# Kernel optimization log

Measured on AMD Instinct MI355X. Metric: run time of the kernel, lower is better.

## Reference

```python
import jax, jax.numpy as jnp
import numpy as np

H, C = 4, 32  # heads, per-head channels
EPS = 1e-5


def setup_inputs() -> dict:
    key = jax.random.key(0)
    ks = jax.random.split(key, 12)
    N, E, IN = 100000, 1600000, 16
    lut_idx = jnp.arange(1024, dtype=jnp.int32)
    x = jax.random.normal(ks[0], (N, IN), dtype=jnp.float32)
    # LUT flag column: exactly the lut_idx nodes have value 1.0 (matches x[:,15]==1.0 mask)
    x = x.at[:, 15].set(0.0).at[lut_idx, 15].set(1.0)
    edge_index = jax.random.randint(ks[1], (2, E), 0, N, dtype=jnp.int64)
    s = 0.1
    return {
        "x": x,
        "edge_index": edge_index,
        "lut_idx": lut_idx,
        "W_lin": jax.random.normal(ks[2], (IN, H * C), dtype=jnp.float32) * s,
        "att_src": jax.random.normal(ks[3], (H, C), dtype=jnp.float32) * s,
        "att_dst": jax.random.normal(ks[4], (H, C), dtype=jnp.float32) * s,
        "bias_gat": jnp.zeros((H * C,), dtype=jnp.float32),
        "gamma": jnp.ones((H * C,), dtype=jnp.float32),
        "beta": jnp.zeros((H * C,), dtype=jnp.float32),
        "W1": jax.random.normal(ks[5], (H * C, 32), dtype=jnp.float32) * s,
        "b1": jnp.zeros((32,), dtype=jnp.float32),
        "W2": jax.random.normal(ks[6], (32, 1), dtype=jnp.float32) * s,
        "b2": jnp.zeros((1,), dtype=jnp.float32),
    }


def gat_conv(x, edge_index, W_lin, att_src, att_dst, bias_gat):
    N = x.shape[0]
    # add self-loops (PyG GATConv default)
    loops = jnp.arange(N, dtype=edge_index.dtype)
    src = jnp.concatenate([edge_index[0], loops])
    dst = jnp.concatenate([edge_index[1], loops])
    h = (x @ W_lin).reshape(N, H, C)                      # [N,H,C]
    a_src = (h * att_src[None]).sum(-1)                   # [N,H]
    a_dst = (h * att_dst[None]).sum(-1)                   # [N,H]
    e = jax.nn.leaky_relu(a_src[src] + a_dst[dst], 0.2)   # [Etot,H]
    m = jax.ops.segment_max(e, dst, num_segments=N)       # stable softmax per dst
    e = jnp.exp(e - m[dst])
    denom = jax.ops.segment_sum(e, dst, num_segments=N)
    alpha = e / denom[dst]                                # [Etot,H]
    msg = h[src] * alpha[:, :, None]                      # [Etot,H,C]
    out = jax.ops.segment_sum(msg, dst, num_segments=N)   # [N,H,C]
    return out.reshape(N, H * C) + bias_gat


def reference(x, edge_index, lut_idx, W_lin, att_src, att_dst, bias_gat,
              gamma, beta, W1, b1, W2, b2):
    h = gat_conv(x, edge_index, W_lin, att_src, att_dst, bias_gat)
    # BatchNorm over nodes (training-mode batch stats, biased var, eps=1e-5)
    mean = h.mean(axis=0)
    var = h.var(axis=0)
    h = (h - mean) / jnp.sqrt(var + EPS) * gamma + beta
    h = jax.nn.relu(h)
    emb = h[lut_idx]                                      # masked LUT nodes
    z = jax.nn.leaky_relu(emb @ W1 + b1, 0.01)            # Dropout is identity in eval
    out = z @ W2 + b2                                     # [n_lut, 1]
    return jnp.squeeze(out, axis=0) if out.shape[0] == 1 else out
```

## Files before the change

kernel.cpp:

```cpp
#include <hip/hip_runtime.h>
#include <hip/hip_fp16.h>
#include <cstdint>
#include <cstring>

typedef unsigned int uint;

#define BSHIFT 8
#define NBUCK 512
#define TILE 4096
#define SCAT_T 512
#define SORT_T 512
#define SORT_CAP 5120

__device__ __forceinline__ float leaky02(float x) { return x > 0.f ? x : 0.2f * x; }
__device__ __forceinline__ float bflo(uint u) { return __uint_as_float(u << 16); }
__device__ __forceinline__ float bfhi(uint u) { return __uint_as_float(u & 0xffff0000u); }

__device__ __forceinline__ uint pack_bf16x2(float a, float b) {
    uint ua = __float_as_uint(a), ub = __float_as_uint(b);
    ua += 0x7fffu + ((ua >> 16) & 1u);
    ub += 0x7fffu + ((ub >> 16) & 1u);
    return (ua >> 16) | (ub & 0xffff0000u);
}

__device__ __forceinline__ uint packh2(float a, float b) {
    __half ha = __float2half_rn(a), hb = __float2half_rn(b);
    unsigned short ua, ub;
    memcpy(&ua, &ha, 2);
    memcpy(&ub, &hb, 2);
    return (uint)ua | ((uint)ub << 16);
}

__global__ void k_prep(const float* __restrict__ W, const float* __restrict__ att_s,
                       const float* __restrict__ att_d, float* __restrict__ WsWd,
                       int* __restrict__ cursor, float* __restrict__ sums,
                       float* __restrict__ sumsq) {
    int t = threadIdx.x;
    cursor[t] = 0; cursor[t + 128] = 0; cursor[t + 256] = 0; cursor[t + 384] = 0;
    sums[t] = 0.f; sumsq[t] = 0.f;
    if (t < 64) {
        int k = t >> 2, hh = t & 3;
        float s1 = 0.f, s2 = 0.f;
        for (int c = 0; c < 32; c++) {
            float wv = W[k * 128 + hh * 32 + c];
            s1 += wv * att_s[hh * 32 + c];
            s2 += wv * att_d[hh * 32 + c];
        }
        WsWd[t] = s1;
        WsWd[64 + t] = s2;
    }
}

__global__ void k_linear(const float* __restrict__ x, const float* __restrict__ W,
                         const float* __restrict__ WsWd,
                         uint* __restrict__ h, float* __restrict__ a_src,
                         float* __restrict__ a_dst, int N) {
    int tid = threadIdx.x;
    __shared__ float sx[32][16];
    __shared__ float sWs[64], sWd[64];
    int j = tid & 63;
    int sub = tid >> 6;
    int n0 = blockIdx.x * 32;

    float2 wreg[16];
#pragma unroll
    for (int k = 0; k < 16; k++) wreg[k] = ((const float2*)(W + k * 128))[j];

    if (tid < 128) {
        int row = tid >> 2;
        if (n0 + row < N)
            ((float4*)sx)[tid] = ((const float4*)(x + (size_t)n0 * 16))[tid];
    } else if (tid < 192) {
        sWs[tid - 128] = WsWd[tid - 128];
    } else {
        sWd[tid - 192] = WsWd[64 + (tid - 192)];
    }
    __syncthreads();

#pragma unroll
    for (int i = 0; i < 8; i++) {
        int loc = sub + i * 4;
        int n = n0 + loc;
        if (n >= N) break;
        float acc0 = 0.f, acc1 = 0.f;
#pragma unroll
        for (int k = 0; k < 16; k++) {
            float xk = sx[loc][k];
            acc0 += xk * wreg[k].x;
            acc1 += xk * wreg[k].y;
        }
        h[(size_t)n * 64 + j] = pack_bf16x2(acc0, acc1);
    }

    int loc2 = tid >> 3, hh = (tid >> 1) & 3, sd = tid & 1;
    int n2 = n0 + loc2;
    if (n2 < N) {
        const float* Wm = sd ? sWd : sWs;
        float acc = 0.f;
#pragma unroll
        for (int k = 0; k < 16; k++) acc += sx[loc2][k] * Wm[k * 4 + hh];
        if (sd) a_dst[n2 * 4 + hh] = acc;
        else    a_src[n2 * 4 + hh] = acc;
    }
}

__global__ void kb_scatter(const int* __restrict__ src, const int* __restrict__ dst, int E,
                           int* __restrict__ cursor, uint* __restrict__ pairs) {
    __shared__ int tileCnt[NBUCK], tileCnt2[NBUCK], tileOff[NBUCK], gbase[NBUCK];
    __shared__ int wsum[8], wbase[8];
    __shared__ uint lp[TILE];
    __shared__ unsigned short lb[TILE];
    int tid = threadIdx.x;
    int l = tid & 63, w = tid >> 6;
    int t0 = blockIdx.x * TILE;
    tileCnt[tid] = 0;
    tileCnt2[tid] = 0;
    __syncthreads();
    int dreg[8], sreg[8];
#pragma unroll
    for (int j = 0; j < 8; j++) {
        int idx = t0 + j * SCAT_T + tid;
        if (idx < E) {
            dreg[j] = dst[idx];
            sreg[j] = src[idx];
            atomicAdd(&tileCnt[dreg[j] >> BSHIFT], 1);
        } else dreg[j] = -1;
    }
    __syncthreads();
    int v = tileCnt[tid];
    int s = v;
#pragma unroll
    for (int off = 1; off < 64; off <<= 1) {
        int t = __shfl_up(s, off);
        if (l >= off) s += t;
    }
    if (l == 63) wsum[w] = s;
    __syncthreads();
    if (tid < 8) {
        int b = 0;
        for (int i = 0; i < tid; i++) b += wsum[i];
        wbase[tid] = b;
    }
    __syncthreads();
    int ex = s - v + wbase[w];
    tileOff[tid] = ex;
    if (v > 0) gbase[tid] = atomicAdd(&cursor[tid], v);
    __syncthreads();
#pragma unroll
    for (int j = 0; j < 8; j++) {
        if (dreg[j] >= 0) {
            int bk = dreg[j] >> BSHIFT;
            int r = atomicAdd(&tileCnt2[bk], 1);
            int pos = tileOff[bk] + r;
            lp[pos] = ((uint)sreg[j] << BSHIFT) | (uint)(dreg[j] & 255);
            lb[pos] = (unsigned short)bk;
        }
    }
    __syncthreads();
    int tot = min(TILE, E - t0);
    for (int k = tid; k < tot; k += SCAT_T) {
        int bk = lb[k];
        int lpos = gbase[bk] + (k - tileOff[bk]);
        if (lpos < SORT_CAP)
            pairs[(size_t)bk * SORT_CAP + lpos] = lp[k];
    }
}

__global__ void kb_sort(const uint* __restrict__ pairs, const int* __restrict__ cursor,
                        const float* __restrict__ a_src, const float* __restrict__ a_dst,
                        int N,
                        int* __restrict__ sorted, uint2* __restrict__ wsorted,
                        int* __restrict__ offsets, int* __restrict__ degs) {
    __shared__ int cnt[256], off0[256];
    __shared__ int wsum[4], wbase[4];
    __shared__ uint lcode[SORT_CAP];
    __shared__ float4 sad[256];
    int tid = threadIdx.x;
    int l = tid & 63, w = tid >> 6;
    int b = blockIdx.x;
    int n0 = b << BSHIFT;
    int nn = min(256, N - n0);
    int ebase = b * SORT_CAP;
    int ecnt = cursor[b];
    if (ecnt > SORT_CAP) ecnt = SORT_CAP;
    if (tid < 256) cnt[tid] = 0;
    if (tid < nn) sad[tid] = ((const float4*)a_dst)[n0 + tid];
    __syncthreads();
    for (int k = tid; k < ecnt; k += SORT_T)
        atomicAdd(&cnt[pairs[ebase + k] & 255], 1);
    __syncthreads();
    int v = (tid < 256) ? cnt[tid] : 0;
    int s = v;
#pragma unroll
    for (int off = 1; off < 64; off <<= 1) {
        int t = __shfl_up(s, off);
        if (l >= off) s += t;
    }
    if (tid < 256 && l == 63) wsum[w] = s;
    __syncthreads();
    if (tid < 4) {
        int base = 0;
        for (int i = 0; i < tid; i++) base += wsum[i];
        wbase[tid] = base;
    }
    __syncthreads();
    if (tid < 256) off0[tid] = s - v + wbase[w];
    __syncthreads();
    if (tid < 256) cnt[tid] = 0;
    __syncthreads();
    for (int k = tid; k < ecnt; k += SORT_T) {
        uint p = pairs[ebase + k];
        int ln = p & 255;
        int r = atomicAdd(&cnt[ln], 1);
        lcode[off0[ln] + r] = p;
    }
    __syncthreads();
    for (int k = tid; k < ecnt; k += SORT_T) {
        uint p = lcode[k];
        int src = (int)(p >> BSHIFT);
        int ln = p & 255;
        sorted[ebase + k] = src;
        float4 as = ((const float4*)a_src)[src];
        float4 ad = sad[ln];
        float w0 = __expf(leaky02(as.x + ad.x));
        float w1 = __expf(leaky02(as.y + ad.y));
        float w2 = __expf(leaky02(as.z + ad.z));
        float w3 = __expf(leaky02(as.w + ad.w));
        wsorted[ebase + k] = make_uint2(packh2(w0, w1), packh2(w2, w3));
    }
    if (tid < nn) {
        offsets[n0 + tid] = ebase + off0[tid];
        degs[n0 + tid] = v;
    }
}

__global__ void k_gat(const int* __restrict__ offsets, const int* __restrict__ degs,
                      const int* __restrict__ sorted, const uint2* __restrict__ wsorted,
                      const uint* __restrict__ h, const float* __restrict__ a_src,
                      const float* __restrict__ a_dst, const float* __restrict__ bias,
                      uint* __restrict__ hagg, int N) {
    int nb = gridDim.x;
    int g = nb >> 3;
    int bi = blockIdx.x;
    int blk = (bi < (g << 3)) ? ((bi & 7) * g + (bi >> 3)) : bi;
    int lane = threadIdx.x & 63;
    int wid = threadIdx.x >> 6;
    int q = lane >> 4;
    int l16 = lane & 15;
    int head = l16 >> 2;
    int d = blk * 16 + wid * 4 + q;
    if (d >= N) return;
    int base = offsets[d];
    int deg = degs[d];

    const int* sp = sorted + base;
    const __half* wp = (const __half*)(wsorted + base) + head;

    float w = __expf(leaky02(a_src[d * 4 + head] + a_dst[d * 4 + head]));
    uint4 u = ((const uint4*)(h + (size_t)d * 64))[l16];
    float sum = w;
    float2 a01 = make_float2(w * bflo(u.x), w * bfhi(u.x));
    float2 a23 = make_float2(w * bflo(u.y), w * bfhi(u.y));
    float2 a45 = make_float2(w * bflo(u.z), w * bfhi(u.z));
    float2 a67 = make_float2(w * bflo(u.w), w * bfhi(u.w));

    int i = 0;
    for (; i + 3 < deg; i += 4) {
        int s0 = sp[i];
        int s1 = sp[i + 1];
        int s2 = sp[i + 2];
        int s3 = sp[i + 3];
        float w0 = __half2float(wp[i * 4]);
        float w1 = __half2float(wp[(i + 1) * 4]);
        float w2 = __half2float(wp[(i + 2) * 4]);
        float w3 = __half2float(wp[(i + 3) * 4]);
        uint4 u0 = ((const uint4*)(h + (size_t)s0 * 64))[l16];
        uint4 u1 = ((const uint4*)(h + (size_t)s1 * 64))[l16];
        uint4 u2 = ((const uint4*)(h + (size_t)s2 * 64))[l16];
        uint4 u3 = ((const uint4*)(h + (size_t)s3 * 64))[l16];
        sum += (w0 + w1) + (w2 + w3);
        float2 w02 = {w0, w0}, w12 = {w1, w1}, w22 = {w2, w2}, w32 = {w3, w3};
        a01 += make_float2(bflo(u0.x), bfhi(u0.x)) * w02
             + make_float2(bflo(u1.x), bfhi(u1.x)) * w12
             + make_float2(bflo(u2.x), bfhi(u2.x)) * w22
             + make_float2(bflo(u3.x), bfhi(u3.x)) * w32;
        a23 += make_float2(bflo(u0.y), bfhi(u0.y)) * w02
             + make_float2(bflo(u1.y), bfhi(u1.y)) * w12
             + make_float2(bflo(u2.y), bfhi(u2.y)) * w22
             + make_float2(bflo(u3.y), bfhi(u3.y)) * w32;
        a45 += make_float2(bflo(u0.z), bfhi(u0.z)) * w02
             + make_float2(bflo(u1.z), bfhi(u1.z)) * w12
             + make_float2(bflo(u2.z), bfhi(u2.z)) * w22
             + make_float2(bflo(u3.z), bfhi(u3.z)) * w32;
        a67 += make_float2(bflo(u0.w), bfhi(u0.w)) * w02
             + make_float2(bflo(u1.w), bfhi(u1.w)) * w12
             + make_float2(bflo(u2.w), bfhi(u2.w)) * w22
             + make_float2(bflo(u3.w), bfhi(u3.w)) * w32;
    }
    for (; i < deg; i++) {
        int s0 = sp[i];
        float w0 = __half2float(wp[i * 4]);
        uint4 u0 = ((const uint4*)(h + (size_t)s0 * 64))[l16];
        sum += w0;
        float2 w02 = {w0, w0};
        a01 += make_float2(bflo(u0.x), bfhi(u0.x)) * w02;
        a23 += make_float2(bflo(u0.y), bfhi(u0.y)) * w02;
        a45 += make_float2(bflo(u0.z), bfhi(u0.z)) * w02;
        a67 += make_float2(bflo(u0.w), bfhi(u0.w)) * w02;
    }
    float inv = 1.f / sum;
    float4 b0 = ((const float4*)bias)[2 * l16];
    float4 b1 = ((const float4*)bias)[2 * l16 + 1];
    uint4 o;
    o.x = pack_bf16x2(a01.x * inv + b0.x, a01.y * inv + b0.y);
    o.y = pack_bf16x2(a23.x * inv + b0.z, a23.y * inv + b0.w);
    o.z = pack_bf16x2(a45.x * inv + b1.x, a45.y * inv + b1.y);
    o.w = pack_bf16x2(a67.x * inv + b1.z, a67.y * inv + b1.w);
    ((uint4*)(hagg + (size_t)d * 64))[l16] = o;
}

__global__ void k_bnstats(const uint* __restrict__ hagg, int N,
                          float* __restrict__ sums, float* __restrict__ sumsq) {
    int t = threadIdx.x;
    int cg = t & 31, rs = t >> 5;
    float4 s = make_float4(0.f, 0.f, 0.f, 0.f), q = make_float4(0.f, 0.f, 0.f, 0.f);
    for (int n = blockIdx.x * 8 + rs; n < N; n += gridDim.x * 8) {
        uint2 u = ((const uint2*)(hagg + (size_t)n * 64))[cg];
        float v0 = bflo(u.x), v1 = bfhi(u.x), v2 = bflo(u.y), v3 = bfhi(u.y);
        s.x += v0; s.y += v1; s.z += v2; s.w += v3;
        q.x += v0 * v0; q.y += v1 * v1; q.z += v2 * v2; q.w += v3 * v3;
    }
    __shared__ float4 ls[256], lq[256];
    ls[t] = s; lq[t] = q;
    __syncthreads();
    if (t < 32) {
        float4 S = ls[t], Q = lq[t];
        for (int r = 1; r < 8; r++) {
            float4 a = ls[t + r * 32], b = lq[t + r * 32];
            S.x += a.x; S.y += a.y; S.z += a.z; S.w += a.w;
            Q.x += b.x; Q.y += b.y; Q.z += b.z; Q.w += b.w;
        }
        atomicAdd(&sums[t * 4 + 0], S.x);
        atomicAdd(&sums[t * 4 + 1], S.y);
        atomicAdd(&sums[t * 4 + 2], S.z);
        atomicAdd(&sums[t * 4 + 3], S.w);
        atomicAdd(&sumsq[t * 4 + 0], Q.x);
        atomicAdd(&sumsq[t * 4 + 1], Q.y);
        atomicAdd(&sumsq[t * 4 + 2], Q.z);
        atomicAdd(&sumsq[t * 4 + 3], Q.w);
    }
}

__global__ void k_mlp(const uint* __restrict__ hagg, const int* __restrict__ lut,
                      const float* __restrict__ sums, const float* __restrict__ sumsq,
                      const float* __restrict__ gamma, const float* __restrict__ beta,
                      const float* __restrict__ W1, const float* __restrict__ b1,
                      const float* __restrict__ W2, const float* __restrict__ b2,
                      float* __restrict__ out, int N, int nlut) {
    int blk = blockIdx.x;
    if (blk >= nlut) return;
    int node = lut[blk];
    int lane = threadIdx.x;
    __shared__ float v[128];
    float invN = 1.f / (float)N;
    uint u = hagg[(size_t)node * 64 + lane];
    int c0 = 2 * lane, c1 = 2 * lane + 1;
    {
        float mean = sums[c0] * invN;
        float var = sumsq[c0] * invN - mean * mean;
        float val = (bflo(u) - mean) / sqrtf(var + 1e-5f) * gamma[c0] + beta[c0];
        v[c0] = fmaxf(val, 0.f);
        mean = sums[c1] * invN;
        var = sumsq[c1] * invN - mean * mean;
        val = (bfhi(u) - mean) / sqrtf(var + 1e-5f) * gamma[c1] + beta[c1];
        v[c1] = fmaxf(val, 0.f);
    }
    __syncthreads();
    float r = 0.f;
    if (lane < 32) {
        float z = b1[lane];
        for (int c = 0; c < 128; c++) z += v[c] * W1[c * 32 + lane];
        z = z > 0.f ? z : 0.01f * z;
        r = z * W2[lane];
    }
#pragma unroll
    for (int off = 16; off >= 1; off >>= 1) r += __shfl_xor(r, off);
    if (lane == 0) out[blk] = r + b2[0];
}

extern "C" void kernel_launch(void* const* d_in, const int* in_sizes, int n_in,
                              void* d_out, int out_size, void* d_ws, size_t ws_size,
                              hipStream_t stream) {
    const float* x     = (const float*)d_in[0];
    const int*   edges = (const int*)d_in[1];
    const int*   lut   = (const int*)d_in[2];
    const float* W_lin = (const float*)d_in[3];
    const float* att_s = (const float*)d_in[4];
    const float* att_d = (const float*)d_in[5];
    const float* bias  = (const float*)d_in[6];
    const float* gamma = (const float*)d_in[7];
    const float* beta  = (const float*)d_in[8];
    const float* W1    = (const float*)d_in[9];
    const float* b1    = (const float*)d_in[10];
    const float* W2    = (const float*)d_in[11];
    const float* b2    = (const float*)d_in[12];

    int N = in_sizes[0] / 16;
    int E = in_sizes[1] / 2;
    int nlut = in_sizes[2];
    int B = (N + 255) >> BSHIFT;

    const int* esrc = edges;
    const int* edst = edges + E;

    char* ws = (char*)d_ws;
    size_t off = 0;
    auto alloc = [&](size_t bytes) -> void* {
        void* p = ws + off;
        off += (bytes + 255) & ~(size_t)255;
        return p;
    };
    uint*  h       = (uint*)alloc((size_t)N * 64 * 4);
    uint*  hagg    = (uint*)alloc((size_t)N * 64 * 4);
    float* a_src   = (float*)alloc((size_t)N * 4 * 4);
    float* a_dst   = (float*)alloc((size_t)N * 4 * 4);
    int*   offsets = (int*)alloc((size_t)N * 4);
    int*   degs    = (int*)alloc((size_t)N * 4);
    int*   sorted  = (int*)alloc((size_t)B * SORT_CAP * 4);
    uint2* wsorted = (uint2*)alloc((size_t)B * SORT_CAP * 8);
    uint*  pairs   = (uint*)alloc((size_t)B * SORT_CAP * 4);
    int*   cursor  = (int*)alloc((size_t)NBUCK * 4);
    float* sums    = (float*)alloc(128 * 4);
    float* sumsq   = (float*)alloc(128 * 4);
    float* WsWd    = (float*)alloc(128 * 4);

    k_prep<<<1, 128, 0, stream>>>(W_lin, att_s, att_d, WsWd, cursor, sums, sumsq);
    k_linear<<<(N + 31) / 32, 256, 0, stream>>>(x, W_lin, WsWd, h, a_src, a_dst, N);
    kb_scatter<<<(E + TILE - 1) / TILE, SCAT_T, 0, stream>>>(esrc, edst, E, cursor, pairs);
    kb_sort<<<B, SORT_T, 0, stream>>>(pairs, cursor, a_src, a_dst, N,
                                      sorted, wsorted, offsets, degs);
    k_gat<<<(N + 15) / 16, 256, 0, stream>>>(offsets, degs, sorted, wsorted, h,
                                             a_src, a_dst, bias, hagg, N);
    k_bnstats<<<256, 256, 0, stream>>>(hagg, N, sums, sumsq);
    k_mlp<<<nlut, 64, 0, stream>>>(hagg, lut, sums, sumsq, gamma, beta, W1, b1, W2, b2,
                                   (float*)d_out, N, nlut);
}
```

Baseline: 237.8 us.

## Recompute attention weights in GAT gather instead of precomputing them in sort

```diff
diff --git a/kernel.cpp b/kernel.cpp
--- a/kernel.cpp
+++ b/kernel.cpp
@@ -1,5 +1,4 @@
 #include <hip/hip_runtime.h>
-#include <hip/hip_fp16.h>
 #include <cstdint>
 #include <cstring>
 
@@ -21,14 +20,6 @@
     ua += 0x7fffu + ((ua >> 16) & 1u);
     ub += 0x7fffu + ((ub >> 16) & 1u);
     return (ua >> 16) | (ub & 0xffff0000u);
-}
-
-__device__ __forceinline__ uint packh2(float a, float b) {
-    __half ha = __float2half_rn(a), hb = __float2half_rn(b);
-    unsigned short ua, ub;
-    memcpy(&ua, &ha, 2);
-    memcpy(&ub, &hb, 2);
-    return (uint)ua | ((uint)ub << 16);
 }
 
 __global__ void k_prep(const float* __restrict__ W, const float* __restrict__ att_s,
@@ -167,14 +158,10 @@
 }
 
 __global__ void kb_sort(const uint* __restrict__ pairs, const int* __restrict__ cursor,
-                        const float* __restrict__ a_src, const float* __restrict__ a_dst,
-                        int N,
-                        int* __restrict__ sorted, uint2* __restrict__ wsorted,
+                        int N, int* __restrict__ sorted,
                         int* __restrict__ offsets, int* __restrict__ degs) {
     __shared__ int cnt[256], off0[256];
     __shared__ int wsum[4], wbase[4];
-    __shared__ uint lcode[SORT_CAP];
-    __shared__ float4 sad[256];
     int tid = threadIdx.x;
     int l = tid & 63, w = tid >> 6;
     int b = blockIdx.x;
@@ -184,7 +171,6 @@
     int ecnt = cursor[b];
     if (ecnt > SORT_CAP) ecnt = SORT_CAP;
     if (tid < 256) cnt[tid] = 0;
-    if (tid < nn) sad[tid] = ((const float4*)a_dst)[n0 + tid];
     __syncthreads();
     for (int k = tid; k < ecnt; k += SORT_T)
         atomicAdd(&cnt[pairs[ebase + k] & 255], 1);
@@ -212,21 +198,7 @@
         uint p = pairs[ebase + k];
         int ln = p & 255;
         int r = atomicAdd(&cnt[ln], 1);
-        lcode[off0[ln] + r] = p;
-    }
-    __syncthreads();
-    for (int k = tid; k < ecnt; k += SORT_T) {
-        uint p = lcode[k];
-        int src = (int)(p >> BSHIFT);
-        int ln = p & 255;
-        sorted[ebase + k] = src;
-        float4 as = ((const float4*)a_src)[src];
-        float4 ad = sad[ln];
-        float w0 = __expf(leaky02(as.x + ad.x));
-        float w1 = __expf(leaky02(as.y + ad.y));
-        float w2 = __expf(leaky02(as.z + ad.z));
-        float w3 = __expf(leaky02(as.w + ad.w));
-        wsorted[ebase + k] = make_uint2(packh2(w0, w1), packh2(w2, w3));
+        sorted[ebase + off0[ln] + r] = (int)(p >> BSHIFT);
     }
     if (tid < nn) {
         offsets[n0 + tid] = ebase + off0[tid];
@@ -234,8 +206,9 @@
     }
 }
 
-__global__ void k_gat(const int* __restrict__ offsets, const int* __restrict__ degs,
-                      const int* __restrict__ sorted, const uint2* __restrict__ wsorted,
+__global__ void __launch_bounds__(256) k_gat(
+                      const int* __restrict__ offsets, const int* __restrict__ degs,
+                      const int* __restrict__ sorted,
                       const uint* __restrict__ h, const float* __restrict__ a_src,
                       const float* __restrict__ a_dst, const float* __restrict__ bias,
                       uint* __restrict__ hagg, int N) {
@@ -254,9 +227,9 @@
     int deg = degs[d];
 
     const int* sp = sorted + base;
-    const __half* wp = (const __half*)(wsorted + base) + head;
-
-    float w = __expf(leaky02(a_src[d * 4 + head] + a_dst[d * 4 + head]));
+
+    float ad = a_dst[d * 4 + head];
+    float w = __expf(leaky02(a_src[d * 4 + head] + ad));
     uint4 u = ((const uint4*)(h + (size_t)d * 64))[l16];
     float sum = w;
     float2 a01 = make_float2(w * bflo(u.x), w * bfhi(u.x));
@@ -265,48 +238,58 @@
     float2 a67 = make_float2(w * bflo(u.w), w * bfhi(u.w));
 
     int i = 0;
+    for (; i + 7 < deg; i += 8) {
+        int ss[8];
+        float as[8];
+        uint4 uu[8];
+#pragma unroll
+        for (int e = 0; e < 8; e++) ss[e] = sp[i + e];
+#pragma unroll
+        for (int e = 0; e < 8; e++) as[e] = a_src[ss[e] * 4 + head];
+#pragma unroll
+        for (int e = 0; e < 8; e++) uu[e] = ((const uint4*)(h + (size_t)ss[e] * 64))[l16];
+#pragma unroll
+        for (int e = 0; e < 8; e++) {
+            float we = __expf(leaky02(as[e] + ad));
+            sum += we;
+            float2 ww = {we, we};
+            a01 += make_float2(bflo(uu[e].x), bfhi(uu[e].x)) * ww;
+            a23 += make_float2(bflo(uu[e].y), bfhi(uu[e].y)) * ww;
+            a45 += make_float2(bflo(uu[e].z), bfhi(uu[e].z)) * ww;
+            a67 += make_float2(bflo(uu[e].w), bfhi(uu[e].w)) * ww;
+        }
+    }
     for (; i + 3 < deg; i += 4) {
-        int s0 = sp[i];
-        int s1 = sp[i + 1];
-        int s2 = sp[i + 2];
-        int s3 = sp[i + 3];
-        float w0 = __half2float(wp[i * 4]);
-        float w1 = __half2float(wp[(i + 1) * 4]);
-        float w2 = __half2float(wp[(i + 2) * 4]);
-        float w3 = __half2float(wp[(i + 3) * 4]);
-        uint4 u0 = ((const uint4*)(h + (size_t)s0 * 64))[l16];
-        uint4 u1 = ((const uint4*)(h + (size_t)s1 * 64))[l16];
-        uint4 u2 = ((const uint4*)(h + (size_t)s2 * 64))[l16];
-        uint4 u3 = ((const uint4*)(h + (size_t)s3 * 64))[l16];
-        sum += (w0 + w1) + (w2 + w3);
-        float2 w02 = {w0, w0}, w12 = {w1, w1}, w22 = {w2, w2}, w32 = {w3, w3};
-        a01 += make_float2(bflo(u0.x), bfhi(u0.x)) * w02
-             + make_float2(bflo(u1.x), bfhi(u1.x)) * w12
-             + make_float2(bflo(u2.x), bfhi(u2.x)) * w22
-             + make_float2(bflo(u3.x), bfhi(u3.x)) * w32;
-        a23 += make_float2(bflo(u0.y), bfhi(u0.y)) * w02
-             + make_float2(bflo(u1.y), bfhi(u1.y)) * w12
-             + make_float2(bflo(u2.y), bfhi(u2.y)) * w22
-             + make_float2(bflo(u3.y), bfhi(u3.y)) * w32;
-        a45 += make_float2(bflo(u0.z), bfhi(u0.z)) * w02
-             + make_float2(bflo(u1.z), bfhi(u1.z)) * w12
-             + make_float2(bflo(u2.z), bfhi(u2.z)) * w22
-             + make_float2(bflo(u3.z), bfhi(u3.z)) * w32;
-        a67 += make_float2(bflo(u0.w), bfhi(u0.w)) * w02
-             + make_float2(bflo(u1.w), bfhi(u1.w)) * w12
-             + make_float2(bflo(u2.w), bfhi(u2.w)) * w22
-             + make_float2(bflo(u3.w), bfhi(u3.w)) * w32;
+        int ss[4];
+        float as[4];
+        uint4 uu[4];
+#pragma unroll
+        for (int e = 0; e < 4; e++) ss[e] = sp[i + e];
+#pragma unroll
+        for (int e = 0; e < 4; e++) as[e] = a_src[ss[e] * 4 + head];
+#pragma unroll
+        for (int e = 0; e < 4; e++) uu[e] = ((const uint4*)(h + (size_t)ss[e] * 64))[l16];
+#pragma unroll
+        for (int e = 0; e < 4; e++) {
+            float we = __expf(leaky02(as[e] + ad));
+            sum += we;
+            float2 ww = {we, we};
+            a01 += make_float2(bflo(uu[e].x), bfhi(uu[e].x)) * ww;
+            a23 += make_float2(bflo(uu[e].y), bfhi(uu[e].y)) * ww;
+            a45 += make_float2(bflo(uu[e].z), bfhi(uu[e].z)) * ww;
+            a67 += make_float2(bflo(uu[e].w), bfhi(uu[e].w)) * ww;
+        }
     }
     for (; i < deg; i++) {
         int s0 = sp[i];
-        float w0 = __half2float(wp[i * 4]);
+        float we = __expf(leaky02(a_src[s0 * 4 + head] + ad));
         uint4 u0 = ((const uint4*)(h + (size_t)s0 * 64))[l16];
-        sum += w0;
-        float2 w02 = {w0, w0};
-        a01 += make_float2(bflo(u0.x), bfhi(u0.x)) * w02;
-        a23 += make_float2(bflo(u0.y), bfhi(u0.y)) * w02;
-        a45 += make_float2(bflo(u0.z), bfhi(u0.z)) * w02;
-        a67 += make_float2(bflo(u0.w), bfhi(u0.w)) * w02;
+        sum += we;
+        float2 ww = {we, we};
+        a01 += make_float2(bflo(u0.x), bfhi(u0.x)) * ww;
+        a23 += make_float2(bflo(u0.y), bfhi(u0.y)) * ww;
+        a45 += make_float2(bflo(u0.z), bfhi(u0.z)) * ww;
+        a67 += make_float2(bflo(u0.w), bfhi(u0.w)) * ww;
     }
     float inv = 1.f / sum;
     float4 b0 = ((const float4*)bias)[2 * l16];
@@ -427,7 +410,6 @@
     int*   offsets = (int*)alloc((size_t)N * 4);
     int*   degs    = (int*)alloc((size_t)N * 4);
     int*   sorted  = (int*)alloc((size_t)B * SORT_CAP * 4);
-    uint2* wsorted = (uint2*)alloc((size_t)B * SORT_CAP * 8);
     uint*  pairs   = (uint*)alloc((size_t)B * SORT_CAP * 4);
     int*   cursor  = (int*)alloc((size_t)NBUCK * 4);
     float* sums    = (float*)alloc(128 * 4);
@@ -437,9 +419,8 @@
     k_prep<<<1, 128, 0, stream>>>(W_lin, att_s, att_d, WsWd, cursor, sums, sumsq);
     k_linear<<<(N + 31) / 32, 256, 0, stream>>>(x, W_lin, WsWd, h, a_src, a_dst, N);
     kb_scatter<<<(E + TILE - 1) / TILE, SCAT_T, 0, stream>>>(esrc, edst, E, cursor, pairs);
-    kb_sort<<<B, SORT_T, 0, stream>>>(pairs, cursor, a_src, a_dst, N,
-                                      sorted, wsorted, offsets, degs);
-    k_gat<<<(N + 15) / 16, 256, 0, stream>>>(offsets, degs, sorted, wsorted, h,
+    kb_sort<<<B, SORT_T, 0, stream>>>(pairs, cursor, N, sorted, offsets, degs);
+    k_gat<<<(N + 15) / 16, 256, 0, stream>>>(offsets, degs, sorted, h,
                                              a_src, a_dst, bias, hagg, N);
     k_bnstats<<<256, 256, 0, stream>>>(hagg, N, sums, sumsq);
     k_mlp<<<nlut, 64, 0, stream>>>(hagg, lut, sums, sumsq, gamma, beta, W1, b1, W2, b2,
```

After: 246.7 us. +3.7%, slower.
